# Kernel optimization log

Hardware: AMD Instinct MI355X
Metric: run time of the kernel (lower is better)

The kernel has to match this reference:

```python
import jax, jax.numpy as jnp
import numpy as np

N, E = 50000, 1_600_000
IN, HID, OUT = 2048, 64, 64


def setup_inputs() -> dict:
    key = jax.random.key(0)
    k1, k2, k3, k4 = jax.random.split(key, 4)
    x = jax.random.normal(k1, (N, IN), dtype=jnp.float32)
    edge_index = jax.random.randint(k2, (2, E), 0, N, dtype=jnp.int64)
    W1 = jax.random.normal(k3, (IN, HID), dtype=jnp.float32) / np.sqrt(IN)
    b1 = jnp.zeros((HID,), dtype=jnp.float32)
    W2 = jax.random.normal(k4, (HID, OUT), dtype=jnp.float32) / np.sqrt(HID)
    b2 = jnp.zeros((OUT,), dtype=jnp.float32)
    return {"x": x, "edge_index": edge_index, "W1": W1, "b1": b1, "W2": W2, "b2": b2}


def gcn_conv(x, edge_index, W, b):
    # PyG GCNConv: h = XW; out = D^{-1/2} (A + I) D^{-1/2} h + b
    n = x.shape[0]
    h = x @ W  # [n, d_out]
    loops = jnp.arange(n, dtype=edge_index.dtype)
    src = jnp.concatenate([edge_index[0], loops])  # [E+n]
    dst = jnp.concatenate([edge_index[1], loops])
    deg = jax.ops.segment_sum(jnp.ones_like(dst, dtype=h.dtype), dst, num_segments=n)
    dinv = jax.lax.rsqrt(deg)  # deg >= 1 because of self-loops
    norm = dinv[src] * dinv[dst]  # [E+n]
    out = jax.ops.segment_sum(h[src] * norm[:, None], dst, num_segments=n)
    return out + b


def reference(x, edge_index, W1, b1, W2, b2):
    h = jax.nn.relu(gcn_conv(x, edge_index, W1, b1))
    h = jax.nn.relu(gcn_conv(h, edge_index, W2, b2))
    return h.mean(axis=0)  # [OUT]
```

## Files before the change

### kernel.cpp

```cpp
#include <hip/hip_runtime.h>
#include <hip/hip_bf16.h>

typedef __attribute__((ext_vector_type(8))) short short8_t;
typedef __attribute__((ext_vector_type(4))) float f32x4;

__device__ __forceinline__ short f2bf(float x){
  union { float f; unsigned u; } v; v.f = x;
  unsigned r = v.u + 0x7fffu + ((v.u >> 16) & 1u);
  return (short)(r >> 16);
}
__device__ __forceinline__ unsigned pack2(float lo, float hi){
  return (unsigned)(unsigned short)f2bf(lo) | ((unsigned)(unsigned short)f2bf(hi) << 16);
}
__device__ __forceinline__ float bf2f(unsigned short u){
  union { unsigned u; float f; } v; v.u = ((unsigned)u) << 16; return v.f;
}

__global__ __launch_bounds__(256) void k_wconv2(const float* __restrict__ W1, short* __restrict__ Wb1,
                                                const float* __restrict__ W2, short* __restrict__ Wb2){
  int tid = blockIdx.x*256 + threadIdx.x;
  const float* W; short* Wb; int t;
  if (tid < 64*2048){ W = W1; Wb = Wb1; t = tid; }
  else if (tid < 64*2048 + 2*2048){ W = W2; Wb = Wb2; t = tid - 64*2048; }
  else return;
  int e  = t & 7;
  int l  = (t >> 3) & 63;
  int nt = (t >> 9) & 3;
  int kt = t >> 11;
  int k  = kt*32 + (l >> 4)*8 + e;
  int col = nt*16 + (l & 15);
  Wb[t] = f2bf(W[(size_t)k*64 + col]);
}

__global__ __launch_bounds__(256) void k_gemm1_hist(const float* __restrict__ A, const short* __restrict__ Wb,
                                                    unsigned short* __restrict__ h1, int M,
                                                    const int* __restrict__ ei, int* __restrict__ cnt,
                                                    int* __restrict__ rank, int E, int GB){
  __shared__ unsigned short lds[4*16*256];
  int b = blockIdx.x;
  int tid = threadIdx.x;
  int wid = tid >> 6, lane = tid & 63;
  int tile = wid >> 1, kh = wid & 1;
  int row0 = b*32 + tile*16;
  int rfrag = lane & 15, grp = lane >> 4;
  char* ldsb = (char*)lds;
  const short8_t* wb = (const short8_t*)Wb + lane;
  f32x4 acc0 = {0.f,0.f,0.f,0.f}, acc1 = acc0, acc2 = acc0, acc3 = acc0;

  int wbase = wid*16*512;
  int wsel  = (lane >> 1);
  int whalf = (lane & 1) << 3;

  for (int ko = 0; ko < 4; ++ko){
    int kcol = kh*1024 + ko*256;
    #pragma unroll
    for (int r = 0; r < 16; ++r){
      int rowc = row0 + r; if (rowc >= M) rowc = M - 1;
      const float4 a = *(const float4*)(A + (size_t)rowc*2048 + kcol + lane*4);
      uint2 p; p.x = pack2(a.x, a.y); p.y = pack2(a.z, a.w);
      *(uint2*)(ldsb + wbase + r*512 + ((wsel ^ (r & 7)) << 4) + whalf) = p;
    }
    asm volatile("s_waitcnt lgkmcnt(0)" ::: "memory");
    #pragma unroll
    for (int kt = 0; kt < 8; ++kt){
      short8_t af = *(const short8_t*)(ldsb + wbase + rfrag*512 + ((((kt<<2) + grp) ^ (rfrag & 7)) << 4));
      int ktg = kh*32 + ko*8 + kt;
      short8_t b0 = wb[(ktg*4+0)*64];
      short8_t b1 = wb[(ktg*4+1)*64];
      short8_t b2 = wb[(ktg*4+2)*64];
      short8_t b3 = wb[(ktg*4+3)*64];
      acc0 = __builtin_amdgcn_mfma_f32_16x16x32_bf16(af, b0, acc0, 0,0,0);
      acc1 = __builtin_amdgcn_mfma_f32_16x16x32_bf16(af, b1, acc1, 0,0,0);
      acc2 = __builtin_amdgcn_mfma_f32_16x16x32_bf16(af, b2, acc2, 0,0,0);
      acc3 = __builtin_amdgcn_mfma_f32_16x16x32_bf16(af, b3, acc3, 0,0,0);
    }
  }

  if (kh == 1){
    float* xch = (float*)(ldsb + wbase);
    *(f32x4*)(xch + lane*20 +  0) = acc0;
    *(f32x4*)(xch + lane*20 +  4) = acc1;
    *(f32x4*)(xch + lane*20 +  8) = acc2;
    *(f32x4*)(xch + lane*20 + 12) = acc3;
  }
  __syncthreads();
  if (kh == 0){
    float* px = (float*)(ldsb + (wid+1)*16*512);
    acc0 += *(const f32x4*)(px + lane*20 +  0);
    acc1 += *(const f32x4*)(px + lane*20 +  4);
    acc2 += *(const f32x4*)(px + lane*20 +  8);
    acc3 += *(const f32x4*)(px + lane*20 + 12);

    int orow = row0 + grp*4;
    unsigned short* op = h1 + (size_t)orow*64 + rfrag;
    #pragma unroll
    for (int reg = 0; reg < 4; ++reg){
      if (orow + reg < M){
        op[reg*64 +  0] = (unsigned short)f2bf(acc0[reg]);
        op[reg*64 + 16] = (unsigned short)f2bf(acc1[reg]);
        op[reg*64 + 32] = (unsigned short)f2bf(acc2[reg]);
        op[reg*64 + 48] = (unsigned short)f2bf(acc3[reg]);
      }
    }
  }

  int per = (E + GB - 1)/GB;
  int lo = b*per, hi = lo + per; if (hi > E) hi = E;
  for (int i = lo + tid; i < hi; i += 256)
    rank[i] = atomicAdd(&cnt[ei[E + i]], 1);
}

__global__ __launch_bounds__(256) void k_part(const int* __restrict__ cnt, int* __restrict__ partial, int N){
  int b = blockIdx.x, t = threadIdx.x;
  int chunk = (N + 255) >> 8;
  int lo = b*chunk, hi = lo + chunk; if (hi > N) hi = N;
  int s = 0;
  for (int i = lo + t; i < hi; i += 256) s += cnt[i];
  __shared__ int sm[256];
  sm[t] = s; __syncthreads();
  for (int d = 128; d; d >>= 1){ if (t < d) sm[t] += sm[t+d]; __syncthreads(); }
  if (t == 0) partial[b] = sm[0];
}

__global__ __launch_bounds__(256) void k_scan2(const int* __restrict__ cnt, const int* __restrict__ partial,
                                               int* __restrict__ off, float* __restrict__ dinv, int N){
  int b = blockIdx.x, t = threadIdx.x;
  __shared__ int ps[256];
  ps[t] = partial[t]; __syncthreads();
  for (int d = 1; d < 256; d <<= 1){
    int v = (t >= d) ? ps[t-d] : 0; __syncthreads(); ps[t] += v; __syncthreads();
  }
  int base  = b ? ps[b-1] : 0;
  int total = ps[255];
  int chunk = (N + 255) >> 8;
  int lo = b*chunk, hi = lo + chunk; if (hi > N) hi = N;
  __shared__ int vs[256];
  int run = base;
  for (int j0 = lo; j0 < hi; j0 += 256){
    int i = j0 + t;
    int c = (i < hi) ? cnt[i] : 0;
    vs[t] = c; __syncthreads();
    for (int d = 1; d < 256; d <<= 1){
      int v = (t >= d) ? vs[t-d] : 0; __syncthreads(); vs[t] += v; __syncthreads();
    }
    if (i < hi){
      off[i] = run + vs[t] - c;
      dinv[i] = rsqrtf((float)(c + 1));
    }
    run += vs[255];
    __syncthreads();
  }
  if (b == 255 && t == 0) off[N] = total;
}

__global__ __launch_bounds__(256) void k_scatter(const int* __restrict__ ei, const int* __restrict__ off,
                                                 const int* __restrict__ rank, int* __restrict__ ebuf, int E){
  int i = blockIdx.x*256 + threadIdx.x;
  if (i < E){
    int s = ei[i], d = ei[E + i];
    ebuf[off[d] + rank[i]] = s;
  }
}

template<int KTILES>
__global__ __launch_bounds__(256) void k_gemm_sm(const unsigned short* __restrict__ Ah,
                                                 const short* __restrict__ Wb,
                                                 unsigned short* __restrict__ out, int M, int lda){
  int wid = threadIdx.x >> 6, lane = threadIdx.x & 63;
  int row0 = (blockIdx.x*4 + wid)*16;
  if (row0 >= M) return;
  int r = lane & 15, g = lane >> 4;
  const short8_t* wb = (const short8_t*)Wb + lane;
  f32x4 acc0 = {0.f,0.f,0.f,0.f}, acc1 = acc0, acc2 = acc0, acc3 = acc0;
  #pragma unroll
  for (int kt = 0; kt < KTILES; ++kt){
    short8_t af = *(const short8_t*)(Ah + (size_t)(row0 + r)*lda + kt*32 + g*8);
    short8_t b0 = wb[(kt*4+0)*64];
    short8_t b1 = wb[(kt*4+1)*64];
    short8_t b2 = wb[(kt*4+2)*64];
    short8_t b3 = wb[(kt*4+3)*64];
    acc0 = __builtin_amdgcn_mfma_f32_16x16x32_bf16(af, b0, acc0, 0,0,0);
    acc1 = __builtin_amdgcn_mfma_f32_16x16x32_bf16(af, b1, acc1, 0,0,0);
    acc2 = __builtin_amdgcn_mfma_f32_16x16x32_bf16(af, b2, acc2, 0,0,0);
    acc3 = __builtin_amdgcn_mfma_f32_16x16x32_bf16(af, b3, acc3, 0,0,0);
  }
  int orow = row0 + g*4;
  unsigned short* op = out + (size_t)orow*64 + r;
  #pragma unroll
  for (int reg = 0; reg < 4; ++reg){
    op[reg*64 +  0] = (unsigned short)f2bf(acc0[reg]);
    op[reg*64 + 16] = (unsigned short)f2bf(acc1[reg]);
    op[reg*64 + 32] = (unsigned short)f2bf(acc2[reg]);
    op[reg*64 + 48] = (unsigned short)f2bf(acc3[reg]);
  }
}

template<bool FUSE>
__global__ __launch_bounds__(256) void k_agg(const unsigned short* __restrict__ hin, const int* __restrict__ off,
                                             const int* __restrict__ ebuf, const float* __restrict__ dinv,
                                             const float* __restrict__ bias, void* __restrict__ outp, int N){
  int lane = threadIdx.x & 63, wid = threadIdx.x >> 6;
  float b = bias[lane];
  float fsum = 0.f;
  int stride = gridDim.x*4;
  for (int i = blockIdx.x*4 + wid; i < N; i += stride){
    float di = dinv[i];
    float acc = di*bf2f(hin[(size_t)i*64 + lane]);
    int j  = off[i];
    int j1 = off[i+1];
    for (; j + 4 <= j1; j += 4){
      int s0 = ebuf[j], s1 = ebuf[j+1], s2 = ebuf[j+2], s3 = ebuf[j+3];
      float w0 = dinv[s0], w1 = dinv[s1], w2 = dinv[s2], w3 = dinv[s3];
      acc += w0*bf2f(hin[(size_t)s0*64 + lane]);
      acc += w1*bf2f(hin[(size_t)s1*64 + lane]);
      acc += w2*bf2f(hin[(size_t)s2*64 + lane]);
      acc += w3*bf2f(hin[(size_t)s3*64 + lane]);
    }
    for (; j < j1; ++j){
      int s = ebuf[j];
      acc += dinv[s]*bf2f(hin[(size_t)s*64 + lane]);
    }
    float z = fmaxf(di*acc + b, 0.f);
    if (FUSE) fsum += z;
    else ((unsigned short*)outp)[(size_t)i*64 + lane] = (unsigned short)f2bf(z);
  }
  if (FUSE){
    __shared__ float sm[4][64];
    sm[wid][lane] = fsum;
    __syncthreads();
    if (wid == 0)
      ((float*)outp)[(size_t)blockIdx.x*64 + lane] = sm[0][lane] + sm[1][lane] + sm[2][lane] + sm[3][lane];
  }
}

__global__ __launch_bounds__(256) void k_final(const float* __restrict__ part, float* __restrict__ out,
                                               int NB, float invN){
  int f = blockIdx.x;
  float s = 0.f;
  for (int b = threadIdx.x; b < NB; b += 256) s += part[(size_t)b*64 + f];
  __shared__ float sm[256];
  sm[threadIdx.x] = s; __syncthreads();
  for (int d = 128; d > 0; d >>= 1){
    if (threadIdx.x < d) sm[threadIdx.x] += sm[threadIdx.x + d];
    __syncthreads();
  }
  if (threadIdx.x == 0) out[f] = sm[0]*invN;
}

extern "C" void kernel_launch(void* const* d_in, const int* in_sizes, int n_in,
                              void* d_out, int out_size, void* d_ws, size_t ws_size,
                              hipStream_t stream){
  const float* x  = (const float*)d_in[0];
  const int*   ei = (const int*)d_in[1];
  const float* W1 = (const float*)d_in[2];
  const float* b1 = (const float*)d_in[3];
  const float* W2 = (const float*)d_in[4];
  const float* b2 = (const float*)d_in[5];
  float* out = (float*)d_out;

  const int IN = 2048;
  int N = in_sizes[0] / IN;
  int E = in_sizes[1] / 2;

  char* w = (char*)d_ws;
  auto alloc = [&](size_t bytes){ char* p = w; w += (bytes + 255) & ~255ULL; return (void*)p; };
  int*   cnt     = (int*)  alloc((size_t)N*4);
  int*   off     = (int*)  alloc((size_t)(N+1)*4);
  float* dinv    = (float*)alloc((size_t)N*4);
  int*   partial = (int*)  alloc(256*4);
  int*   rank    = (int*)  alloc((size_t)E*4);
  int*   ebuf    = (int*)  alloc((size_t)E*4);
  short* Wb1     = (short*)alloc((size_t)64*2048*2);
  short* Wb2     = (short*)alloc((size_t)2*2048*2);
  unsigned short* h1 = (unsigned short*)alloc((size_t)N*64*2);
  unsigned short* z1 = (unsigned short*)alloc((size_t)N*64*2);
  const int NB2 = 2048;
  float* part    = (float*)alloc((size_t)NB2*64*4);

  int EB = (E + 255)/256;
  int GB = (N + 31)/32;
  int smblocks = ((N + 15)/16 + 3)/4;

  hipMemsetAsync(cnt, 0, (size_t)N*4, stream);
  k_wconv2 <<<(64*2048 + 2*2048 + 255)/256, 256, 0, stream>>>(W1, Wb1, W2, Wb2);
  k_gemm1_hist<<<GB, 256, 0, stream>>>(x, Wb1, h1, N, ei, cnt, rank, E, GB);
  k_part   <<<256, 256, 0, stream>>>(cnt, partial, N);
  k_scan2  <<<256, 256, 0, stream>>>(cnt, partial, off, dinv, N);
  k_scatter<<<EB, 256, 0, stream>>>(ei, off, rank, ebuf, E);
  k_agg<false><<<NB2, 256, 0, stream>>>(h1, off, ebuf, dinv, b1, (void*)z1, N);
  k_gemm_sm<2><<<smblocks, 256, 0, stream>>>(z1, Wb2, h1, N, 64);
  k_agg<true> <<<NB2, 256, 0, stream>>>(h1, off, ebuf, dinv, b2, (void*)part, N);
  k_final  <<<64, 256, 0, stream>>>(part, out, NB2, 1.0f/(float)N);
}
```

Before: 363.3 us.

## Drop split-K in layer-1 GEMM, shard degree histogram, widen aggregation unroll

The first GEMM now gives each wave the full K range over 64 rows per block. It issues eight float4 row loads in a batch before packing to LDS, which removes the cross-wave LDS reduction and the barrier and raises memory-level parallelism on the large fp32 input read. The degree histogram is split into 16 shards chosen by block index, with per-shard scatter bases computed in the scan, to reduce atomic contention. The cost is a 16x larger memset and extra reads. The edge range per block is now fixed at 2048 edges, so edge coverage relies on E being no larger than the grid size times 2048. The aggregation inner loop is unrolled to 8 neighbours to keep more gathers in flight, and a row-bounds guard is added to the small GEMM.

```diff
diff --git a/kernel.cpp b/kernel.cpp
--- a/kernel.cpp
+++ b/kernel.cpp
@@ -32,16 +32,14 @@
   Wb[t] = f2bf(W[(size_t)k*64 + col]);
 }
 
-__global__ __launch_bounds__(256) void k_gemm1_hist(const float* __restrict__ A, const short* __restrict__ Wb,
-                                                    unsigned short* __restrict__ h1, int M,
-                                                    const int* __restrict__ ei, int* __restrict__ cnt,
-                                                    int* __restrict__ rank, int E, int GB){
-  __shared__ unsigned short lds[4*16*256];
-  int b = blockIdx.x;
-  int tid = threadIdx.x;
+__global__ __launch_bounds__(256, 4) void k_gemm1_hist(const float* __restrict__ A, const short* __restrict__ Wb,
+                                                       unsigned short* __restrict__ h1, int M,
+                                                       const int* __restrict__ ei, int* __restrict__ cnt16,
+                                                       int* __restrict__ rank, int E, int N){
+  __shared__ unsigned short lds[64*256];
+  int b = blockIdx.x, tid = threadIdx.x;
   int wid = tid >> 6, lane = tid & 63;
-  int tile = wid >> 1, kh = wid & 1;
-  int row0 = b*32 + tile*16;
+  int row0 = b*64 + wid*16;
   int rfrag = lane & 15, grp = lane >> 4;
   char* ldsb = (char*)lds;
   const short8_t* wb = (const short8_t*)Wb + lane;
@@ -51,20 +49,34 @@
   int wsel  = (lane >> 1);
   int whalf = (lane & 1) << 3;
 
-  for (int ko = 0; ko < 4; ++ko){
-    int kcol = kh*1024 + ko*256;
-    #pragma unroll
-    for (int r = 0; r < 16; ++r){
-      int rowc = row0 + r; if (rowc >= M) rowc = M - 1;
-      const float4 a = *(const float4*)(A + (size_t)rowc*2048 + kcol + lane*4);
-      uint2 p; p.x = pack2(a.x, a.y); p.y = pack2(a.z, a.w);
+  const float* rowp[16];
+  #pragma unroll
+  for (int r = 0; r < 16; ++r){
+    int rowc = row0 + r; if (rowc >= M) rowc = M - 1;
+    rowp[r] = A + (size_t)rowc*2048 + lane*4;
+  }
+
+  for (int ko = 0; ko < 8; ++ko){
+    float4 fv[8];
+    #pragma unroll
+    for (int r = 0; r < 8; ++r) fv[r] = *(const float4*)(rowp[r] + ko*256);
+    #pragma unroll
+    for (int r = 0; r < 8; ++r){
+      uint2 p; p.x = pack2(fv[r].x, fv[r].y); p.y = pack2(fv[r].z, fv[r].w);
       *(uint2*)(ldsb + wbase + r*512 + ((wsel ^ (r & 7)) << 4) + whalf) = p;
+    }
+    #pragma unroll
+    for (int r = 0; r < 8; ++r) fv[r] = *(const float4*)(rowp[8 + r] + ko*256);
+    #pragma unroll
+    for (int r = 0; r < 8; ++r){
+      uint2 p; p.x = pack2(fv[r].x, fv[r].y); p.y = pack2(fv[r].z, fv[r].w);
+      *(uint2*)(ldsb + wbase + (8 + r)*512 + ((wsel ^ ((8 + r) & 7)) << 4) + whalf) = p;
     }
     asm volatile("s_waitcnt lgkmcnt(0)" ::: "memory");
     #pragma unroll
     for (int kt = 0; kt < 8; ++kt){
       short8_t af = *(const short8_t*)(ldsb + wbase + rfrag*512 + ((((kt<<2) + grp) ^ (rfrag & 7)) << 4));
-      int ktg = kh*32 + ko*8 + kt;
+      int ktg = ko*8 + kt;
       short8_t b0 = wb[(ktg*4+0)*64];
       short8_t b1 = wb[(ktg*4+1)*64];
       short8_t b2 = wb[(ktg*4+2)*64];
@@ -76,54 +88,42 @@
     }
   }
 
-  if (kh == 1){
-    float* xch = (float*)(ldsb + wbase);
-    *(f32x4*)(xch + lane*20 +  0) = acc0;
-    *(f32x4*)(xch + lane*20 +  4) = acc1;
-    *(f32x4*)(xch + lane*20 +  8) = acc2;
-    *(f32x4*)(xch + lane*20 + 12) = acc3;
-  }
-  __syncthreads();
-  if (kh == 0){
-    float* px = (float*)(ldsb + (wid+1)*16*512);
-    acc0 += *(const f32x4*)(px + lane*20 +  0);
-    acc1 += *(const f32x4*)(px + lane*20 +  4);
-    acc2 += *(const f32x4*)(px + lane*20 +  8);
-    acc3 += *(const f32x4*)(px + lane*20 + 12);
-
-    int orow = row0 + grp*4;
-    unsigned short* op = h1 + (size_t)orow*64 + rfrag;
-    #pragma unroll
-    for (int reg = 0; reg < 4; ++reg){
-      if (orow + reg < M){
-        op[reg*64 +  0] = (unsigned short)f2bf(acc0[reg]);
-        op[reg*64 + 16] = (unsigned short)f2bf(acc1[reg]);
-        op[reg*64 + 32] = (unsigned short)f2bf(acc2[reg]);
-        op[reg*64 + 48] = (unsigned short)f2bf(acc3[reg]);
-      }
-    }
-  }
-
-  int per = (E + GB - 1)/GB;
-  int lo = b*per, hi = lo + per; if (hi > E) hi = E;
+  int orow = row0 + grp*4;
+  unsigned short* op = h1 + (size_t)orow*64 + rfrag;
+  #pragma unroll
+  for (int reg = 0; reg < 4; ++reg){
+    if (orow + reg < M){
+      op[reg*64 +  0] = (unsigned short)f2bf(acc0[reg]);
+      op[reg*64 + 16] = (unsigned short)f2bf(acc1[reg]);
+      op[reg*64 + 32] = (unsigned short)f2bf(acc2[reg]);
+      op[reg*64 + 48] = (unsigned short)f2bf(acc3[reg]);
+    }
+  }
+
+  int lo = b << 11, hi = lo + 2048; if (hi > E) hi = E;
+  int* cs = cnt16 + (size_t)(b & 15)*N;
   for (int i = lo + tid; i < hi; i += 256)
-    rank[i] = atomicAdd(&cnt[ei[E + i]], 1);
-}
-
-__global__ __launch_bounds__(256) void k_part(const int* __restrict__ cnt, int* __restrict__ partial, int N){
+    rank[i] = atomicAdd(&cs[ei[E + i]], 1);
+}
+
+__global__ __launch_bounds__(256) void k_part(const int* __restrict__ cnt16, int* __restrict__ partial, int N){
   int b = blockIdx.x, t = threadIdx.x;
   int chunk = (N + 255) >> 8;
   int lo = b*chunk, hi = lo + chunk; if (hi > N) hi = N;
   int s = 0;
-  for (int i = lo + t; i < hi; i += 256) s += cnt[i];
+  for (int i = lo + t; i < hi; i += 256){
+    #pragma unroll
+    for (int sh = 0; sh < 16; ++sh) s += cnt16[(size_t)sh*N + i];
+  }
   __shared__ int sm[256];
   sm[t] = s; __syncthreads();
   for (int d = 128; d; d >>= 1){ if (t < d) sm[t] += sm[t+d]; __syncthreads(); }
   if (t == 0) partial[b] = sm[0];
 }
 
-__global__ __launch_bounds__(256) void k_scan2(const int* __restrict__ cnt, const int* __restrict__ partial,
-                                               int* __restrict__ off, float* __restrict__ dinv, int N){
+__global__ __launch_bounds__(256) void k_scan2(const int* __restrict__ cnt16, const int* __restrict__ partial,
+                                               int* __restrict__ off, int* __restrict__ sbase,
+                                               float* __restrict__ dinv, int N){
   int b = blockIdx.x, t = threadIdx.x;
   __shared__ int ps[256];
   ps[t] = partial[t]; __syncthreads();
@@ -138,14 +138,22 @@
   int run = base;
   for (int j0 = lo; j0 < hi; j0 += 256){
     int i = j0 + t;
-    int c = (i < hi) ? cnt[i] : 0;
-    vs[t] = c; __syncthreads();
+    int cs[16]; int c = 0;
+    if (i < hi){
+      #pragma unroll
+      for (int sh = 0; sh < 16; ++sh){ cs[sh] = cnt16[(size_t)sh*N + i]; c += cs[sh]; }
+    }
+    vs[t] = (i < hi) ? c : 0; __syncthreads();
     for (int d = 1; d < 256; d <<= 1){
       int v = (t >= d) ? vs[t-d] : 0; __syncthreads(); vs[t] += v; __syncthreads();
     }
     if (i < hi){
-      off[i] = run + vs[t] - c;
+      int excl = run + vs[t] - c;
+      off[i] = excl;
       dinv[i] = rsqrtf((float)(c + 1));
+      int runs = excl;
+      #pragma unroll
+      for (int sh = 0; sh < 16; ++sh){ sbase[(size_t)sh*N + i] = runs; runs += cs[sh]; }
     }
     run += vs[255];
     __syncthreads();
@@ -153,12 +161,14 @@
   if (b == 255 && t == 0) off[N] = total;
 }
 
-__global__ __launch_bounds__(256) void k_scatter(const int* __restrict__ ei, const int* __restrict__ off,
-                                                 const int* __restrict__ rank, int* __restrict__ ebuf, int E){
+__global__ __launch_bounds__(256) void k_scatter(const int* __restrict__ ei, const int* __restrict__ sbase,
+                                                 const int* __restrict__ rank, int* __restrict__ ebuf,
+                                                 int E, int N){
   int i = blockIdx.x*256 + threadIdx.x;
   if (i < E){
     int s = ei[i], d = ei[E + i];
-    ebuf[off[d] + rank[i]] = s;
+    int sh = (i >> 11) & 15;
+    ebuf[sbase[(size_t)sh*N + d] + rank[i]] = s;
   }
 }
 
@@ -188,10 +198,12 @@
   unsigned short* op = out + (size_t)orow*64 + r;
   #pragma unroll
   for (int reg = 0; reg < 4; ++reg){
-    op[reg*64 +  0] = (unsigned short)f2bf(acc0[reg]);
-    op[reg*64 + 16] = (unsigned short)f2bf(acc1[reg]);
-    op[reg*64 + 32] = (unsigned short)f2bf(acc2[reg]);
-    op[reg*64 + 48] = (unsigned short)f2bf(acc3[reg]);
+    if (orow + reg < M){
+      op[reg*64 +  0] = (unsigned short)f2bf(acc0[reg]);
+      op[reg*64 + 16] = (unsigned short)f2bf(acc1[reg]);
+      op[reg*64 + 32] = (unsigned short)f2bf(acc2[reg]);
+      op[reg*64 + 48] = (unsigned short)f2bf(acc3[reg]);
+    }
   }
 }
 
@@ -208,13 +220,20 @@
     float acc = di*bf2f(hin[(size_t)i*64 + lane]);
     int j  = off[i];
     int j1 = off[i+1];
-    for (; j + 4 <= j1; j += 4){
-      int s0 = ebuf[j], s1 = ebuf[j+1], s2 = ebuf[j+2], s3 = ebuf[j+3];
+    for (; j + 8 <= j1; j += 8){
+      int s0 = ebuf[j],   s1 = ebuf[j+1], s2 = ebuf[j+2], s3 = ebuf[j+3];
+      int s4 = ebuf[j+4], s5 = ebuf[j+5], s6 = ebuf[j+6], s7 = ebuf[j+7];
       float w0 = dinv[s0], w1 = dinv[s1], w2 = dinv[s2], w3 = dinv[s3];
-      acc += w0*bf2f(hin[(size_t)s0*64 + lane]);
-      acc += w1*bf2f(hin[(size_t)s1*64 + lane]);
-      acc += w2*bf2f(hin[(size_t)s2*64 + lane]);
-      acc += w3*bf2f(hin[(size_t)s3*64 + lane]);
+      float w4 = dinv[s4], w5 = dinv[s5], w6 = dinv[s6], w7 = dinv[s7];
+      float h0 = bf2f(hin[(size_t)s0*64 + lane]);
+      float h1v = bf2f(hin[(size_t)s1*64 + lane]);
+      float h2 = bf2f(hin[(size_t)s2*64 + lane]);
+      float h3 = bf2f(hin[(size_t)s3*64 + lane]);
+      float h4 = bf2f(hin[(size_t)s4*64 + lane]);
+      float h5 = bf2f(hin[(size_t)s5*64 + lane]);
+      float h6 = bf2f(hin[(size_t)s6*64 + lane]);
+      float h7 = bf2f(hin[(size_t)s7*64 + lane]);
+      acc += w0*h0 + w1*h1v + w2*h2 + w3*h3 + w4*h4 + w5*h5 + w6*h6 + w7*h7;
     }
     for (; j < j1; ++j){
       int s = ebuf[j];
@@ -264,8 +283,9 @@
 
   char* w = (char*)d_ws;
   auto alloc = [&](size_t bytes){ char* p = w; w += (bytes + 255) & ~255ULL; return (void*)p; };
-  int*   cnt     = (int*)  alloc((size_t)N*4);
+  int*   cnt16   = (int*)  alloc((size_t)16*N*4);
   int*   off     = (int*)  alloc((size_t)(N+1)*4);
+  int*   sbase   = (int*)  alloc((size_t)16*N*4);
   float* dinv    = (float*)alloc((size_t)N*4);
   int*   partial = (int*)  alloc(256*4);
   int*   rank    = (int*)  alloc((size_t)E*4);
@@ -278,15 +298,15 @@
   float* part    = (float*)alloc((size_t)NB2*64*4);
 
   int EB = (E + 255)/256;
-  int GB = (N + 31)/32;
+  int GB = (N + 63)/64;
   int smblocks = ((N + 15)/16 + 3)/4;
 
-  hipMemsetAsync(cnt, 0, (size_t)N*4, stream);
+  hipMemsetAsync(cnt16, 0, (size_t)16*N*4, stream);
   k_wconv2 <<<(64*2048 + 2*2048 + 255)/256, 256, 0, stream>>>(W1, Wb1, W2, Wb2);
-  k_gemm1_hist<<<GB, 256, 0, stream>>>(x, Wb1, h1, N, ei, cnt, rank, E, GB);
-  k_part   <<<256, 256, 0, stream>>>(cnt, partial, N);
-  k_scan2  <<<256, 256, 0, stream>>>(cnt, partial, off, dinv, N);
-  k_scatter<<<EB, 256, 0, stream>>>(ei, off, rank, ebuf, E);
+  k_gemm1_hist<<<GB, 256, 0, stream>>>(x, Wb1, h1, N, ei, cnt16, rank, E, N);
+  k_part   <<<256, 256, 0, stream>>>(cnt16, partial, N);
+  k_scan2  <<<256, 256, 0, stream>>>(cnt16, partial, off, sbase, dinv, N);
+  k_scatter<<<EB, 256, 0, stream>>>(ei, sbase, rank, ebuf, E, N);
   k_agg<false><<<NB2, 256, 0, stream>>>(h1, off, ebuf, dinv, b1, (void*)z1, N);
   k_gemm_sm<2><<<smblocks, 256, 0, stream>>>(z1, Wb2, h1, N, 64);
   k_agg<true> <<<NB2, 256, 0, stream>>>(h1, off, ebuf, dinv, b2, (void*)part, N);
```

Result: faster. 347.7 us (-4.3%).
